# Kernel optimization log

Hardware: AMD Instinct MI355X
Metric: run time of the kernel (lower is better)

## Reference

```python
import jax, jax.numpy as jnp
import numpy as np

LX, LY = 256, 256
K_CLASSES = 4
N_SWEEPS = 2
N_SITES = LX * LY

# 8-neighborhood offsets (Moore neighborhood), border handled by clipping
_OFFSETS = np.array([[-1, -1], [-1, 0], [-1, 1],
                     [0, -1],           [0, 1],
                     [1, -1],  [1, 0],  [1, 1]], dtype=np.int32)


def setup_inputs() -> dict:
    key = jax.random.key(0)
    k1, k2, k3, k4 = jax.random.split(key, 4)
    X_init = jax.random.randint(k1, (LX, LY), 0, K_CLASSES).astype(jnp.int32)
    perm = jax.random.permutation(k2, jnp.arange(N_SITES)).astype(jnp.int32)
    uniforms = jax.random.uniform(k3, (N_SWEEPS, N_SITES), dtype=jnp.float32)
    beta = jax.random.uniform(k4, (), dtype=jnp.float32) + 0.5  # Potts coupling
    return {"X_init": X_init, "perm": perm, "uniforms": uniforms,
            "beta": beta, "K": K_CLASSES}


def reference(X_init, perm, uniforms, beta, K):
    lx, ly = X_init.shape
    off = jnp.asarray(_OFFSETS)              # (8, 2)
    classes = jnp.arange(K)                  # (K,)

    def update_one_site(X, uv, r):
        u, v = jnp.unravel_index(uv, (lx, ly))
        uu = jnp.clip(u + off[:, 0], 0, lx - 1)   # (8,) neighbor rows
        vv = jnp.clip(v + off[:, 1], 0, ly - 1)   # (8,) neighbor cols
        neigh = X[uu, vv]                          # (8,) dynamic gather
        # Potts potential: p_k proportional to exp(beta * #{neighbors == k})
        counts = (neigh[None, :] == classes[:, None]).sum(axis=1)  # (K,)
        probs = jax.nn.softmax(beta * counts.astype(jnp.float32))  # (K,) sums to 1
        # inverse-CDF categorical sample, as in the original cumsum < r
        x_sample = jnp.count_nonzero(jnp.cumsum(probs) < r)
        return X.at[u, v].set(x_sample.astype(X.dtype))  # scatter write

    def one_sweep(X, rs):
        def body(Xc, inp):
            uv, r = inp
            return update_one_site(Xc, uv, r), None
        X, _ = jax.lax.scan(body, X, (perm, rs))
        return X, None

    X_final, _ = jax.lax.scan(one_sweep, X_init, uniforms)  # N_SWEEPS sweeps
    return X_final
```

## Files before the change

kernel.cpp:

```cpp
#include <hip/hip_runtime.h>
#include <math.h>

#define NSITES 65536
#define WIN 4096
#define NW 16
#define RMAX 64


__device__ __forceinline__ int agg_pos(int v, int* c, int vmax) {
  int pos = 0;
  const int lane = threadIdx.x & 63;
  for (int vv = 1; vv <= vmax; ++vv) {
    unsigned long long m = __ballot(v == vv);
    if (m) {
      int leader = __ffsll((long long)m) - 1;
      int base = 0;
      if (lane == leader) base = atomicAdd(&c[vv], (int)__popcll(m));
      base = __shfl(base, leader);
      if (v == vv) pos = base + (int)__popcll(m & ((1ull << lane) - 1ull));
    }
  }
  return pos;
}

__global__ __launch_bounds__(1024) void GibbsSched_kernel(
    const int* __restrict__ perm, const float* __restrict__ uni,
    uint2* __restrict__ recpk, int* __restrict__ ends) {
  __shared__ unsigned short posg[NSITES];
  __shared__ unsigned short lvl[WIN];
  __shared__ int cnt[RMAX + 1], coff[RMAX + 1];
  __shared__ int chg, bmax;
  const int tid = threadIdx.x;
  const int w = blockIdx.x;
  const int wbase = w * WIN;

  for (int g = tid; g < NSITES / 8; g += 1024)
    ((uint4*)posg)[g] = make_uint4(0u, 0u, 0u, 0u);
  for (int i = tid; i <= RMAX; i += 1024) { cnt[i] = 0; coff[i] = 0; }
  if (tid == 0) bmax = 0;
  __syncthreads();

  int uvk[4];
#pragma unroll
  for (int k = 0; k < 4; ++k) {
    const int lt = tid + k * 1024;
    uvk[k] = perm[wbase + lt];
    posg[uvk[k]] = (unsigned short)(lt + 1);
  }
  __syncthreads();

  unsigned short pred[4][8];
  int myl[4];
#pragma unroll
  for (int k = 0; k < 4; ++k) {
    const int lt = tid + k * 1024;
    const int uv = uvk[k], u = uv >> 8, v = uv & 255;
    const int um = u ? u - 1 : 0, up = u < 255 ? u + 1 : 255;
    const int vm = v ? v - 1 : 0, vp = v < 255 ? v + 1 : 255;
    const int nb8[8] = {(um << 8) | vm, (um << 8) | v, (um << 8) | vp,
                        (u << 8) | vm,                 (u << 8) | vp,
                        (up << 8) | vm, (up << 8) | v, (up << 8) | vp};
#pragma unroll
    for (int j = 0; j < 8; ++j) {
      const int p = posg[nb8[j]];
      pred[k][j] = (p && p - 1 < lt) ? (unsigned short)(p - 1)
                                     : (unsigned short)0xFFFF;
    }
    lvl[lt] = 1;
    myl[k] = 1;
  }
  __syncthreads();

  for (int pass = 0; pass < 128; ++pass) {
    if (tid == 0) chg = 0;
    __syncthreads();
    bool ch = false;
#pragma unroll
    for (int k = 0; k < 4; ++k) {
      int m = 0;
#pragma unroll
      for (int j = 0; j < 8; ++j) {
        const unsigned short p = pred[k][j];
        if (p != 0xFFFF) m = max(m, (int)lvl[p]);
      }
      const int nl = m + 1;
      if (nl != myl[k]) {
        myl[k] = nl;
        lvl[tid + k * 1024] = (unsigned short)nl;
        ch = true;
      }
    }
    if (ch) chg = 1;
    __syncthreads();
    if (chg == 0) break;
  }

#pragma unroll
  for (int k = 0; k < 4; ++k) atomicMax(&bmax, myl[k]);
  __syncthreads();
  const int vmax = bmax;

#pragma unroll
  for (int k = 0; k < 4; ++k) (void)agg_pos(myl[k], cnt, vmax);
  __syncthreads();
  if (tid == 0) {
    int e = 0;
    for (int r = 0; r < RMAX; ++r) {
      coff[r] = e;
      e += cnt[r];
      ends[w * RMAX + r] = e;
    }
  }
  __syncthreads();

#pragma unroll
  for (int k = 0; k < 4; ++k) {
    const int pos = agg_pos(myl[k], coff, vmax);
    const int lt = tid + k * 1024;
    const int gp = wbase + pos;
    recpk[gp] = make_uint2((unsigned)uvk[k],
                           __float_as_uint(uni[wbase + lt]));
    recpk[NSITES + gp] = make_uint2((unsigned)uvk[k],
                                    __float_as_uint(uni[NSITES + wbase + lt]));
  }
}

__device__ __forceinline__ void do_update(unsigned char* cell,
                                          const unsigned int* cellw,
                                          const float4* ctab, unsigned uvv,
                                          float r) {
  const int u = uvv >> 8, v = (int)(uvv & 255u);
  const int um = u ? u - 1 : 0, up = u < 255 ? u + 1 : 255;
  const int vm = v ? v - 1 : 0, vp = v < 255 ? v + 1 : 255;
  const int cb = vm >> 2;
  const int sh0 = (vm & 3) << 3;
  const int shv = (v - vm) << 3;
  const int shp = (vp - vm) << 3;
  int acc = 0;
  {
    const unsigned int* rw = cellw + (um << 6) + cb;
    const unsigned long long wd =
        ((unsigned long long)rw[1] << 32) | (unsigned long long)rw[0];
    const unsigned wl = (unsigned)(wd >> sh0);
    acc += 1 << ((wl & 255u) << 2);
    acc += 1 << (((wl >> shv) & 255u) << 2);
    acc += 1 << (((wl >> shp) & 255u) << 2);
  }
  {
    const unsigned int* rw = cellw + (u << 6) + cb;
    const unsigned long long wd =
        ((unsigned long long)rw[1] << 32) | (unsigned long long)rw[0];
    const unsigned wl = (unsigned)(wd >> sh0);
    acc += 1 << ((wl & 255u) << 2);
    acc += 1 << (((wl >> shp) & 255u) << 2);
  }
  {
    const unsigned int* rw = cellw + (up << 6) + cb;
    const unsigned long long wd =
        ((unsigned long long)rw[1] << 32) | (unsigned long long)rw[0];
    const unsigned wl = (unsigned)(wd >> sh0);
    acc += 1 << ((wl & 255u) << 2);
    acc += 1 << (((wl >> shv) & 255u) << 2);
    acc += 1 << (((wl >> shp) & 255u) << 2);
  }
  const int n0 = acc & 15, n1 = (acc >> 4) & 15, n2 = (acc >> 8) & 15;
  const float4 c = ctab[n0 + 9 * n1 + 81 * n2];
  int cnt = (c.x < r) ? 1 : 0;
  cnt += (c.y < r) ? 1 : 0;
  cnt += (c.z < r) ? 1 : 0;
  cnt += (c.w < r) ? 1 : 0;
  cell[uvv] = (unsigned char)cnt;
}

__global__ __launch_bounds__(1024) void GibbsSampler_90443421319469_kernel(
    const int* __restrict__ Xi, const uint2* __restrict__ recpk,
    const float* __restrict__ betap, const int* __restrict__ ends,
    int* __restrict__ out) {
#pragma clang fp contract(off)
  __shared__ __align__(16) unsigned int cellw[NSITES / 4];
  __shared__ float4 ctab[732];
  __shared__ int lend[NW * RMAX];
  unsigned char* cell = (unsigned char*)cellw;
  const int tid = threadIdx.x;
  const float beta = betap[0];

  for (int g = tid; g < NSITES / 4; g += 1024) {
    int4 x = ((const int4*)Xi)[g];
    cellw[g] = (unsigned)(x.x & 255) | ((unsigned)(x.y & 255) << 8) |
               ((unsigned)(x.z & 255) << 16) | ((unsigned)(x.w & 255) << 24);
  }
  lend[tid] = ends[tid];
  for (int t = tid; t < 729; t += 1024) {
    const int n0 = t % 9, n1 = (t / 9) % 9, n2 = t / 81;
    const int n3 = 8 - n0 - n1 - n2;
    float4 val = make_float4(2.f, 2.f, 2.f, 2.f);
    if (n3 >= 0) {
      const int mx = max(max(n0, n1), max(n2, n3));
      const float xm = beta * (float)mx;
      const float x0 = beta * (float)n0;
      const float x1 = beta * (float)n1;
      const float x2 = beta * (float)n2;
      const float x3 = beta * (float)n3;
      const float e0 = (float)exp((double)(x0 - xm));
      const float e1 = (float)exp((double)(x1 - xm));
      const float e2 = (float)exp((double)(x2 - xm));
      const float e3 = (float)exp((double)(x3 - xm));
      const float s = ((e0 + e1) + e2) + e3;
      const float c0 = e0 / s;
      const float c1 = c0 + e1 / s;
      const float c2 = c1 + e2 / s;
      const float c3 = c2 + e3 / s;
      val = make_float4(c0, c1, c2, c3);
    }
    ctab[t] = val;
  }
  __syncthreads();

  for (int w = 0; w < 2 * NW; ++w) {
    const int ww = w & (NW - 1);
    const int sw = w >> 4;
    const uint2* rp = recpk + sw * NSITES + ww * WIN;
    const int* le = &lend[ww * RMAX];

    int nb = 0, ne = le[1];
    uint2 cur = make_uint2(0u, 0u);
    if (tid < ne) cur = rp[tid];

    for (int rd = 1; rd < RMAX; ++rd) {
      const int b = nb, e = ne;
      if (b >= WIN) break;
      nb = e;
      ne = (rd + 1 < RMAX) ? le[rd + 1] : e;
      uint2 nxt = make_uint2(0u, 0u);
      if (nb + tid < ne) nxt = rp[nb + tid];
      if (b + tid < e) do_update(cell, cellw, ctab, cur.x, __uint_as_float(cur.y));
      for (int i = b + tid + 1024; i < e; i += 1024) {
        const uint2 rc = rp[i];
        do_update(cell, cellw, ctab, rc.x, __uint_as_float(rc.y));
      }
      __syncthreads();
      cur = nxt;
    }
  }

  for (int g = tid; g < NSITES / 4; g += 1024) {
    const unsigned p = cellw[g];
    int4 o;
    o.x = (int)(p & 255u);
    o.y = (int)((p >> 8) & 255u);
    o.z = (int)((p >> 16) & 255u);
    o.w = (int)((p >> 24) & 255u);
    ((int4*)out)[g] = o;
  }
}

extern "C" void kernel_launch(void* const* d_in, const int* in_sizes, int n_in,
                              void* d_out, int out_size, void* d_ws,
                              size_t ws_size, hipStream_t stream) {
  const int* Xi = (const int*)d_in[0];
  const int* perm = (const int*)d_in[1];
  const float* uni = (const float*)d_in[2];
  const float* beta = (const float*)d_in[3];
  int* out = (int*)d_out;

  char* ws = (char*)d_ws;
  uint2* recpk = (uint2*)ws;
  int* ends = (int*)(ws + 2 * NSITES * 8);

  GibbsSched_kernel<<<dim3(NW), dim3(1024), 0, stream>>>(perm, uni, recpk,
                                                         ends);
  GibbsSampler_90443421319469_kernel<<<dim3(1), dim3(1024), 0, stream>>>(
      Xi, recpk, beta, ends, out);
}
```

Baseline: 229.4 us.

## Use larger scheduling windows, finish short level tails within one wavefront

Halves the number of scheduling windows by doubling window size to 8192 sites, so the single-block sampler runs fewer window passes and fewer block-wide barriers per sweep. When 64 or fewer sites remain in a window, one wavefront processes all remaining dependency levels in order without __syncthreads. The level computation compacts predecessor lists into packed 16-bit pairs and skips sites that have no predecessors. The CDF table is split into four scalar arrays instead of float4. Larger windows raise per-thread register use in the scheduler and may produce deeper level chains.

```diff
diff --git a/kernel.cpp b/kernel.cpp
--- a/kernel.cpp
+++ b/kernel.cpp
@@ -2,8 +2,9 @@
 #include <math.h>
 
 #define NSITES 65536
-#define WIN 4096
-#define NW 16
+#define WIN 8192
+#define NW 8
+#define KN 8
 #define RMAX 64
 
 
@@ -40,19 +41,19 @@
   if (tid == 0) bmax = 0;
   __syncthreads();
 
-  int uvk[4];
-#pragma unroll
-  for (int k = 0; k < 4; ++k) {
+  int uvk[KN];
+#pragma unroll
+  for (int k = 0; k < KN; ++k) {
     const int lt = tid + k * 1024;
     uvk[k] = perm[wbase + lt];
     posg[uvk[k]] = (unsigned short)(lt + 1);
   }
   __syncthreads();
 
-  unsigned short pred[4][8];
-  int myl[4];
-#pragma unroll
-  for (int k = 0; k < 4; ++k) {
+  unsigned int predp[KN][4];
+  int myl[KN];
+#pragma unroll
+  for (int k = 0; k < KN; ++k) {
     const int lt = tid + k * 1024;
     const int uv = uvk[k], u = uv >> 8, v = uv & 255;
     const int um = u ? u - 1 : 0, up = u < 255 ? u + 1 : 255;
@@ -60,12 +61,17 @@
     const int nb8[8] = {(um << 8) | vm, (um << 8) | v, (um << 8) | vp,
                         (u << 8) | vm,                 (u << 8) | vp,
                         (up << 8) | vm, (up << 8) | v, (up << 8) | vp};
+    unsigned short pl[8];
+    int np = 0;
 #pragma unroll
     for (int j = 0; j < 8; ++j) {
       const int p = posg[nb8[j]];
-      pred[k][j] = (p && p - 1 < lt) ? (unsigned short)(p - 1)
-                                     : (unsigned short)0xFFFF;
-    }
+      if (p && p - 1 < lt) pl[np++] = (unsigned short)(p - 1);
+    }
+    for (int j = np; j < 8; ++j) pl[j] = 0xFFFF;
+#pragma unroll
+    for (int j = 0; j < 4; ++j)
+      predp[k][j] = (unsigned)pl[2 * j] | ((unsigned)pl[2 * j + 1] << 16);
     lvl[lt] = 1;
     myl[k] = 1;
   }
@@ -76,12 +82,15 @@
     __syncthreads();
     bool ch = false;
 #pragma unroll
-    for (int k = 0; k < 4; ++k) {
+    for (int k = 0; k < KN; ++k) {
+      if (predp[k][0] == 0xFFFFFFFFu) continue;
       int m = 0;
 #pragma unroll
-      for (int j = 0; j < 8; ++j) {
-        const unsigned short p = pred[k][j];
-        if (p != 0xFFFF) m = max(m, (int)lvl[p]);
+      for (int j = 0; j < 4; ++j) {
+        const unsigned pk = predp[k][j];
+        const unsigned lo = pk & 0xFFFFu, hi = pk >> 16;
+        if (lo != 0xFFFFu) m = max(m, (int)lvl[lo]);
+        if (hi != 0xFFFFu) m = max(m, (int)lvl[hi]);
       }
       const int nl = m + 1;
       if (nl != myl[k]) {
@@ -96,12 +105,12 @@
   }
 
 #pragma unroll
-  for (int k = 0; k < 4; ++k) atomicMax(&bmax, myl[k]);
+  for (int k = 0; k < KN; ++k) atomicMax(&bmax, myl[k]);
   __syncthreads();
   const int vmax = bmax;
 
 #pragma unroll
-  for (int k = 0; k < 4; ++k) (void)agg_pos(myl[k], cnt, vmax);
+  for (int k = 0; k < KN; ++k) (void)agg_pos(myl[k], cnt, vmax);
   __syncthreads();
   if (tid == 0) {
     int e = 0;
@@ -114,7 +123,7 @@
   __syncthreads();
 
 #pragma unroll
-  for (int k = 0; k < 4; ++k) {
+  for (int k = 0; k < KN; ++k) {
     const int pos = agg_pos(myl[k], coff, vmax);
     const int lt = tid + k * 1024;
     const int gp = wbase + pos;
@@ -127,8 +136,9 @@
 
 __device__ __forceinline__ void do_update(unsigned char* cell,
                                           const unsigned int* cellw,
-                                          const float4* ctab, unsigned uvv,
-                                          float r) {
+                                          const float* c0a, const float* c1a,
+                                          const float* c2a, const float* c3a,
+                                          unsigned uvv, float r) {
   const int u = uvv >> 8, v = (int)(uvv & 255u);
   const int um = u ? u - 1 : 0, up = u < 255 ? u + 1 : 255;
   const int vm = v ? v - 1 : 0, vp = v < 255 ? v + 1 : 255;
@@ -164,11 +174,11 @@
     acc += 1 << (((wl >> shp) & 255u) << 2);
   }
   const int n0 = acc & 15, n1 = (acc >> 4) & 15, n2 = (acc >> 8) & 15;
-  const float4 c = ctab[n0 + 9 * n1 + 81 * n2];
-  int cnt = (c.x < r) ? 1 : 0;
-  cnt += (c.y < r) ? 1 : 0;
-  cnt += (c.z < r) ? 1 : 0;
-  cnt += (c.w < r) ? 1 : 0;
+  const int idx = n0 + 9 * n1 + 81 * n2;
+  int cnt = (c0a[idx] < r) ? 1 : 0;
+  cnt += (c1a[idx] < r) ? 1 : 0;
+  cnt += (c2a[idx] < r) ? 1 : 0;
+  cnt += (c3a[idx] < r) ? 1 : 0;
   cell[uvv] = (unsigned char)cnt;
 }
 
@@ -178,7 +188,7 @@
     int* __restrict__ out) {
 #pragma clang fp contract(off)
   __shared__ __align__(16) unsigned int cellw[NSITES / 4];
-  __shared__ float4 ctab[732];
+  __shared__ float c0a[729], c1a[729], c2a[729], c3a[729];
   __shared__ int lend[NW * RMAX];
   unsigned char* cell = (unsigned char*)cellw;
   const int tid = threadIdx.x;
@@ -189,11 +199,11 @@
     cellw[g] = (unsigned)(x.x & 255) | ((unsigned)(x.y & 255) << 8) |
                ((unsigned)(x.z & 255) << 16) | ((unsigned)(x.w & 255) << 24);
   }
-  lend[tid] = ends[tid];
+  if (tid < NW * RMAX) lend[tid] = ends[tid];
   for (int t = tid; t < 729; t += 1024) {
     const int n0 = t % 9, n1 = (t / 9) % 9, n2 = t / 81;
     const int n3 = 8 - n0 - n1 - n2;
-    float4 val = make_float4(2.f, 2.f, 2.f, 2.f);
+    float v0 = 2.f, v1 = 2.f, v2 = 2.f, v3 = 2.f;
     if (n3 >= 0) {
       const int mx = max(max(n0, n1), max(n2, n3));
       const float xm = beta * (float)mx;
@@ -206,19 +216,18 @@
       const float e2 = (float)exp((double)(x2 - xm));
       const float e3 = (float)exp((double)(x3 - xm));
       const float s = ((e0 + e1) + e2) + e3;
-      const float c0 = e0 / s;
-      const float c1 = c0 + e1 / s;
-      const float c2 = c1 + e2 / s;
-      const float c3 = c2 + e3 / s;
-      val = make_float4(c0, c1, c2, c3);
-    }
-    ctab[t] = val;
+      v0 = e0 / s;
+      v1 = v0 + e1 / s;
+      v2 = v1 + e2 / s;
+      v3 = v2 + e3 / s;
+    }
+    c0a[t] = v0; c1a[t] = v1; c2a[t] = v2; c3a[t] = v3;
   }
   __syncthreads();
 
   for (int w = 0; w < 2 * NW; ++w) {
     const int ww = w & (NW - 1);
-    const int sw = w >> 4;
+    const int sw = w >> 3;
     const uint2* rp = recpk + sw * NSITES + ww * WIN;
     const int* le = &lend[ww * RMAX];
 
@@ -229,14 +238,42 @@
     for (int rd = 1; rd < RMAX; ++rd) {
       const int b = nb, e = ne;
       if (b >= WIN) break;
+
+      if (WIN - b <= 64) {
+        if (tid < 64) {
+          const int i = b + tid;
+          int myrd = 0;
+          uint2 rc = make_uint2(0u, 0u);
+          if (i < WIN) {
+            myrd = rd;
+            while (le[myrd] <= i) ++myrd;
+            rc = rp[i];
+          }
+          int mx = myrd;
+#pragma unroll
+          for (int off = 1; off < 64; off <<= 1)
+            mx = max(mx, __shfl_xor(mx, off));
+          for (int rr = rd; rr <= mx; ++rr) {
+            if (myrd == rr)
+              do_update(cell, cellw, c0a, c1a, c2a, c3a, rc.x,
+                        __uint_as_float(rc.y));
+          }
+        }
+        __syncthreads();
+        break;
+      }
+
       nb = e;
       ne = (rd + 1 < RMAX) ? le[rd + 1] : e;
       uint2 nxt = make_uint2(0u, 0u);
       if (nb + tid < ne) nxt = rp[nb + tid];
-      if (b + tid < e) do_update(cell, cellw, ctab, cur.x, __uint_as_float(cur.y));
+      if (b + tid < e)
+        do_update(cell, cellw, c0a, c1a, c2a, c3a, cur.x,
+                  __uint_as_float(cur.y));
       for (int i = b + tid + 1024; i < e; i += 1024) {
         const uint2 rc = rp[i];
-        do_update(cell, cellw, ctab, rc.x, __uint_as_float(rc.y));
+        do_update(cell, cellw, c0a, c1a, c2a, c3a, rc.x,
+                  __uint_as_float(rc.y));
       }
       __syncthreads();
       cur = nxt;
```

Measured after the change: 267.3 us. +16.5%, slower.
